# Kernel tuning notes

Measured on AMD Instinct MI355X. Metric: run time of the kernel, lower is better.

Reference implementation:

```python
import jax, jax.numpy as jnp
import numpy as np

D = 1024      # total input features
R = 32        # number of ragged regions
RMAX = 32     # max region size (padding target)
HIDDEN = [128, 128]
H1, H2 = HIDDEN
B = 8192      # batch size


def _made_masks(r, rmax, hidden):
    """TFP AutoregressiveNetwork masks (left-to-right order, 'equal' hidden degrees,
    params=2, use_bias=False), zero-padded to rmax features."""
    order = np.arange(1, r + 1)
    degs = [order]
    for u in hidden:
        mn = min(int(degs[-1].min()), r - 1)
        degs.append(np.maximum(mn, np.ceil(np.arange(1, u + 1) * (r - 1) / float(u + 1)).astype(np.int64)))
    m1 = np.zeros((rmax, hidden[0]), bool)
    m1[:r] = degs[0][:, None] <= degs[1][None, :]
    m2 = degs[1][:, None] <= degs[2][None, :]
    mout = np.zeros((hidden[-1], rmax * 2), bool)
    out_deg = np.repeat(order, 2)  # output layout is feature-major: [feat, param]
    mout[:, :2 * r] = degs[-1][:, None] < out_deg[None, :]
    return m1, m2, mout


def setup_inputs() -> dict:
    rng = np.random.default_rng(0)
    perm = rng.permutation(D)
    sizes = rng.integers(8, RMAX + 1, size=R)
    idx = np.zeros((R, RMAX), np.int64)
    valid = np.zeros((R, RMAX), bool)
    M1 = np.zeros((R, RMAX, H1), bool)
    M2 = np.zeros((R, H1, H2), bool)
    Mout = np.zeros((R, H2, RMAX * 2), bool)
    pos = 0
    for i in range(R):
        s = int(sizes[i])
        idx[i, :s] = perm[pos:pos + s]
        pos += s
        valid[i, :s] = True
        M1[i], M2[i], Mout[i] = _made_masks(s, RMAX, HIDDEN)
    key = jax.random.key(0)
    k1, k2, k3, k4 = jax.random.split(key, 4)
    inputs = jax.random.normal(k1, (B, D), jnp.float32)
    W1 = jax.random.normal(k2, (R, RMAX, H1), jnp.float32) / np.float32(np.sqrt(RMAX))
    W2 = jax.random.normal(k3, (R, H1, H2), jnp.float32) / np.float32(np.sqrt(H1))
    Wout = jax.random.normal(k4, (R, H2, RMAX * 2), jnp.float32) / np.float32(np.sqrt(H2))
    return {"inputs": inputs, "W1": W1, "W2": W2, "Wout": Wout,
            "idx": jnp.asarray(idx), "valid": jnp.asarray(valid),
            "M1": jnp.asarray(M1), "M2": jnp.asarray(M2), "Mout": jnp.asarray(Mout)}


def reference(inputs, W1, W2, Wout, idx, valid, M1, M2, Mout):
    f = inputs.dtype
    v = valid.astype(f)                              # [R, RMAX]
    xg = jnp.take(inputs, idx, axis=1) * v           # [B, R, RMAX] ragged gather (padded)
    # MADE masked MLP (relu, no bias), batched over all regions at once
    h1 = jax.nn.relu(jnp.einsum('brd,rdh->brh', xg, W1 * M1.astype(f)))
    h2 = jax.nn.relu(jnp.einsum('brh,rhk->brk', h1, W2 * M2.astype(f)))
    out = jnp.einsum('brk,rko->bro', h2, Wout * Mout.astype(f))
    out = out.reshape(out.shape[0], out.shape[1], RMAX, 2)
    shift, log_s = out[..., 0], out[..., 1]
    # MAF inverse: u = (x - shift) * exp(-log_scale); logdet = -sum(log_scale)
    u = (xg - shift) * jnp.exp(-log_s)
    elem = -0.5 * u * u - 0.5 * jnp.log(2.0 * jnp.pi) - log_s
    ll = jnp.sum(elem * v, axis=-1)                  # [B, R]
    return ll[..., None]                             # [B, R, 1] as in tf.stack of expand_dims
```

## Files before the change

### kernel.cpp

```cpp
#include <hip/hip_runtime.h>
#include <math.h>


#define RR 32
#define DD 1024
#define HH 128
#define OO 64
#define TROWS 64
#define TILES 8
#define BLOCKS_PER_R 16

#define SHP 136
#define SXG 40
#define SSC 136

typedef _Float16 f16x8_t __attribute__((ext_vector_type(8)));
typedef float f32x4_t __attribute__((ext_vector_type(4)));
typedef unsigned short u16;
typedef unsigned int u32;

__device__ __forceinline__ u32 pkrtz(float a, float b) {
    union { __fp16 v __attribute__((ext_vector_type(2))); u32 u; } c;
    c.v = __builtin_amdgcn_cvt_pkrtz(a, b);
    return c.u;
}
__device__ __forceinline__ f32x4_t mfma16h(f16x8_t a, f16x8_t b, f32x4_t c) {
    return __builtin_amdgcn_mfma_f32_16x16x32_f16(a, b, c, 0, 0, 0);
}

__device__ __forceinline__ void stage_block16(const float* __restrict__ W,
                                              const int* __restrict__ M,
                                              int ldc, int c0, int K, u16* dst,
                                              int tid)
{
    const int kb = tid >> 3;
    const int cb = tid & 7;
    if (kb * 4 >= K) return;
    const int k0 = kb * 4;
    float e[4][4];
#pragma unroll
    for (int i = 0; i < 4; ++i) {
        const int o = ((k0 + i) * ldc + c0 + 4 * cb) >> 2;
        float4 w = ((const float4*)W)[o];
        int4   m = ((const int4*)M)[o];
        e[i][0] = m.x ? w.x : 0.f; e[i][1] = m.y ? w.y : 0.f;
        e[i][2] = m.z ? w.z : 0.f; e[i][3] = m.w ? w.w : 0.f;
    }
#pragma unroll
    for (int j = 0; j < 4; ++j) {
        uint2 p;
        p.x = pkrtz(e[0][j], e[1][j]);
        p.y = pkrtz(e[2][j], e[3][j]);
        *(uint2*)&dst[(4 * cb + j) * SSC + k0] = p;
    }
}

__device__ __forceinline__ void relu_store16(u16* __restrict__ dst, int o, f32x4_t a)
{
    uint2 s;
    s.x = pkrtz(fmaxf(a[0], 0.f), fmaxf(a[1], 0.f));
    s.y = pkrtz(fmaxf(a[2], 0.f), fmaxf(a[3], 0.f));
    *(uint2*)&dst[o] = s;
}

__global__ __launch_bounds__(512, 4)
void made_flow_r26(const float* __restrict__ inputs,
                   const float* __restrict__ W1,
                   const float* __restrict__ W2,
                   const float* __restrict__ Wout,
                   const int* __restrict__ idx,
                   const int* __restrict__ valid,
                   const int* __restrict__ M1,
                   const int* __restrict__ M2,
                   const int* __restrict__ Mout,
                   float* __restrict__ out)
{
    __shared__ __align__(16) u16 h1s[TROWS * SHP];
    __shared__ __align__(16) u16 h2s[TROWS * SHP];
    __shared__ __align__(16) u16 wout_lds[OO * SSC];
    __shared__ __align__(16) u16 xgh[2][TROWS * SXG];
    __shared__ __align__(16) float red2[2][TROWS][4];
    __shared__ int   idx_s[RR];
    __shared__ float v_s[RR];

    u16* const scr  = h1s;
    u16* const scr2 = h2s;

    const int tid  = threadIdx.x;
    const int r    = blockIdx.x / BLOCKS_PER_R;
    const int rb   = blockIdx.x % BLOCKS_PER_R;
    const int ts64 = rb * TILES * TROWS;

    const int lane = tid & 63;
    const int wave = tid >> 6;
    const int q    = lane >> 4;
    const int l16  = lane & 15;
    const int mq   = wave & 3;
    const int nh   = wave >> 2;
    const int wm3  = wave & 3;
    const int ni3  = wave >> 2;

    if (tid < RR) {
        idx_s[tid] = idx[r * RR + tid];
        v_s[tid]   = valid[r * RR + tid] ? 1.f : 0.f;
    }

    f16x8_t a1[2];
    f16x8_t a2[2][4];
    {
        const float* W1r = W1 + r * RR * HH;   const int* M1r = M1 + r * RR * HH;
        const float* W2r = W2 + r * HH * HH;   const int* M2r = M2 + r * HH * HH;
        const float* Wor = Wout + r * HH * OO; const int* Mor = Mout + r * HH * OO;
        for (int i = 0; i < 2; ++i) {
            __syncthreads();
            if (tid < 256) stage_block16(W2r, M2r, HH, 32 * (2 * i),     HH, scr,  tid);
            else           stage_block16(W2r, M2r, HH, 32 * (2 * i + 1), HH, scr2, tid - 256);
            __syncthreads();
            if (mq == 2 * i) {
#pragma unroll
                for (int mi = 0; mi < 2; ++mi)
#pragma unroll
                    for (int ks = 0; ks < 4; ++ks)
                        a2[mi][ks] = *(const f16x8_t*)&scr[(16 * mi + l16) * SSC + ks * 32 + q * 8];
            } else if (mq == 2 * i + 1) {
#pragma unroll
                for (int mi = 0; mi < 2; ++mi)
#pragma unroll
                    for (int ks = 0; ks < 4; ++ks)
                        a2[mi][ks] = *(const f16x8_t*)&scr2[(16 * mi + l16) * SSC + ks * 32 + q * 8];
            }
        }
        for (int i = 0; i < 2; ++i) {
            __syncthreads();
            if (tid < 256) stage_block16(W1r, M1r, HH, 32 * (2 * i),     RR, scr,  tid);
            else           stage_block16(W1r, M1r, HH, 32 * (2 * i + 1), RR, scr2, tid - 256);
            __syncthreads();
            if (mq == 2 * i) {
#pragma unroll
                for (int mi = 0; mi < 2; ++mi)
                    a1[mi] = *(const f16x8_t*)&scr [(16 * mi + l16) * SSC + q * 8];
            } else if (mq == 2 * i + 1) {
#pragma unroll
                for (int mi = 0; mi < 2; ++mi)
                    a1[mi] = *(const f16x8_t*)&scr2[(16 * mi + l16) * SSC + q * 8];
            }
        }
        if (tid < 256) stage_block16(Wor, Mor, OO, 0,  HH, wout_lds,            tid);
        else           stage_block16(Wor, Mor, OO, 32, HH, wout_lds + 32 * SSC, tid - 256);
    }
    __syncthreads();

    const f32x4_t zero4 = {0.f, 0.f, 0.f, 0.f};
    const int grow = tid >> 4;
    const int gg   = tid & 15;
    const int   ci0 = idx_s[2 * gg], ci1 = idx_s[2 * gg + 1];
    const float cv0 = v_s[2 * gg],   cv1 = v_s[2 * gg + 1];
    const int j0  = 8 * wm3 + 2 * q;
    const float vj0 = v_s[j0], vj1 = v_s[j0 + 1];
    const int gb0 = (ts64 + grow) * DD;
    const int gb1 = (ts64 + 32 + grow) * DD;

    float gx[4];
    {
        float a0 = inputs[gb0 + ci0] * cv0, a1v = inputs[gb0 + ci1] * cv1;
        float b0 = inputs[gb1 + ci0] * cv0, b1v = inputs[gb1 + ci1] * cv1;
        *(u32*)&xgh[0][grow * SXG + 2 * gg]        = pkrtz(a0, a1v);
        *(u32*)&xgh[0][(grow + 32) * SXG + 2 * gg] = pkrtz(b0, b1v);
        gx[0] = inputs[gb0 + TROWS * DD + ci0] * cv0;
        gx[1] = inputs[gb0 + TROWS * DD + ci1] * cv1;
        gx[2] = inputs[gb1 + TROWS * DD + ci0] * cv0;
        gx[3] = inputs[gb1 + TROWS * DD + ci1] * cv1;
    }
    __syncthreads();

    {
#pragma unroll
        for (int nn = 0; nn < 2; ++nn) {
            const int rw = 16 * (2 * nh + nn) + l16;
            f16x8_t b = *(const f16x8_t*)&xgh[0][rw * SXG + q * 8];
#pragma unroll
            for (int mi = 0; mi < 2; ++mi) {
                f32x4_t a = mfma16h(a1[mi], b, zero4);
                relu_store16(h1s, rw * SHP + 32 * mq + 16 * mi + 4 * q, a);
            }
        }
    }

    for (int t = 0; t < TILES; ++t) {
        __syncthreads();

        const bool dg = (t + 1 < TILES);

        if (dg) {
            *(u32*)&xgh[(t + 1) & 1][grow * SXG + 2 * gg]        = pkrtz(gx[0], gx[1]);
            *(u32*)&xgh[(t + 1) & 1][(grow + 32) * SXG + 2 * gg] = pkrtz(gx[2], gx[3]);
        }
        if (t + 2 < TILES) {
            const int base = (t + 2) * (TROWS * DD);
            gx[0] = inputs[gb0 + base + ci0] * cv0;
            gx[1] = inputs[gb0 + base + ci1] * cv1;
            gx[2] = inputs[gb1 + base + ci0] * cv0;
            gx[3] = inputs[gb1 + base + ci1] * cv1;
        }
        {
            f32x4_t acc[2][2] = {{zero4, zero4}, {zero4, zero4}};
            __builtin_amdgcn_s_setprio(1);
#pragma unroll
            for (int ks = 0; ks < 4; ++ks) {
#pragma unroll
                for (int nn = 0; nn < 2; ++nn) {
                    f16x8_t b = *(const f16x8_t*)&h1s[(16 * (2 * nh + nn) + l16) * SHP + ks * 32 + q * 8];
#pragma unroll
                    for (int mi = 0; mi < 2; ++mi)
                        acc[mi][nn] = mfma16h(a2[mi][ks], b, acc[mi][nn]);
                }
            }
            __builtin_amdgcn_s_setprio(0);
#pragma unroll
            for (int mi = 0; mi < 2; ++mi)
#pragma unroll
                for (int nn = 0; nn < 2; ++nn)
                    relu_store16(h2s, (16 * (2 * nh + nn) + l16) * SHP + 32 * mq + 16 * mi + 4 * q,
                                 acc[mi][nn]);
        }
        if (t >= 2 && tid < TROWS) {
            float4 rv = *(const float4*)&red2[t & 1][tid][0];
            out[((rb * TILES + (t - 2)) * TROWS + tid) * RR + r] =
                rv.x + rv.y + rv.z + rv.w;
        }
        __syncthreads();

        f32x4_t acc3[2] = {zero4, zero4};
        __builtin_amdgcn_s_setprio(1);
#pragma unroll
        for (int ks = 0; ks < 4; ++ks) {
            f16x8_t ao = *(const f16x8_t*)&wout_lds[(16 * wm3 + l16) * SSC + ks * 32 + q * 8];
#pragma unroll
            for (int nn = 0; nn < 2; ++nn) {
                f16x8_t b = *(const f16x8_t*)&h2s[(16 * (ni3 + 2 * nn) + l16) * SHP + ks * 32 + q * 8];
                acc3[nn] = mfma16h(ao, b, acc3[nn]);
            }
        }
        __builtin_amdgcn_s_setprio(0);

        if (dg) {
#pragma unroll
            for (int nn = 0; nn < 2; ++nn) {
                const int rw = 16 * (2 * nh + nn) + l16;
                f16x8_t b = *(const f16x8_t*)&xgh[(t + 1) & 1][rw * SXG + q * 8];
#pragma unroll
                for (int mi = 0; mi < 2; ++mi) {
                    f32x4_t a = mfma16h(a1[mi], b, zero4);
                    relu_store16(h1s, rw * SHP + 32 * mq + 16 * mi + 4 * q, a);
                }
            }
        }

#pragma unroll
        for (int nn = 0; nn < 2; ++nn) {
            const int row = 16 * (ni3 + 2 * nn) + l16;
            u32 xw = *(const u32*)&xgh[t & 1][row * SXG + j0];
            union { u32 u; _Float16 h[2]; } xc; xc.u = xw;
            const float xv0 = (float)xc.h[0], xv1 = (float)xc.h[1];
            f32x4_t a = acc3[nn];
            const float u0 = (xv0 - a[0]) * __expf(-a[1]);
            const float u1 = (xv1 - a[2]) * __expf(-a[3]);
            float p = (-0.5f * u0 * u0 - 0.91893853320467266954f - a[1]) * vj0
                    + (-0.5f * u1 * u1 - 0.91893853320467266954f - a[3]) * vj1;
            p += __shfl_xor(p, 16, 64);
            p += __shfl_xor(p, 32, 64);
            if (q == 0) red2[t & 1][row][wm3] = p;
        }
    }

    __syncthreads();
    if (tid < 2 * TROWS) {
        const int tt  = TILES - 2 + (tid >> 6);
        const int row = tid & 63;
        float4 rv = *(const float4*)&red2[tt & 1][row][0];
        out[((rb * TILES + tt) * TROWS + row) * RR + r] =
            rv.x + rv.y + rv.z + rv.w;
    }
}

extern "C" void kernel_launch(void* const* d_in, const int* in_sizes, int n_in,
                              void* d_out, int out_size, void* d_ws, size_t ws_size,
                              hipStream_t stream)
{
    const float* inputs = (const float*)d_in[0];
    const float* W1     = (const float*)d_in[1];
    const float* W2     = (const float*)d_in[2];
    const float* Wout   = (const float*)d_in[3];
    const int*   idx    = (const int*)d_in[4];
    const int*   valid  = (const int*)d_in[5];
    const int*   M1     = (const int*)d_in[6];
    const int*   M2     = (const int*)d_in[7];
    const int*   Mout   = (const int*)d_in[8];
    float*       out    = (float*)d_out;

    hipLaunchKernelGGL(made_flow_r26, dim3(RR * BLOCKS_PER_R), dim3(512), 0, stream,
                       inputs, W1, W2, Wout, idx, valid, M1, M2, Mout, out);
}
```

Before: 118.9 us.

## Restructure weight staging prologue and hoist gathers ahead of weight loads

```diff
diff --git a/kernel.cpp b/kernel.cpp
--- a/kernel.cpp
+++ b/kernel.cpp
@@ -13,6 +13,7 @@
 #define SHP 136
 #define SXG 40
 #define SSC 136
+#define SW1 40
 
 typedef _Float16 f16x8_t __attribute__((ext_vector_type(8)));
 typedef float f32x4_t __attribute__((ext_vector_type(4)));
@@ -30,11 +31,11 @@
 
 __device__ __forceinline__ void stage_block16(const float* __restrict__ W,
                                               const int* __restrict__ M,
-                                              int ldc, int c0, int K, u16* dst,
-                                              int tid)
+                                              int ldc, int c0, int K,
+                                              u16* dst, int sd, int tp)
 {
-    const int kb = tid >> 3;
-    const int cb = tid & 7;
+    const int kb = tp >> 3;
+    const int cb = tp & 7;
     if (kb * 4 >= K) return;
     const int k0 = kb * 4;
     float e[4][4];
@@ -51,7 +52,7 @@
         uint2 p;
         p.x = pkrtz(e[0][j], e[1][j]);
         p.y = pkrtz(e[2][j], e[3][j]);
-        *(uint2*)&dst[(4 * cb + j) * SSC + k0] = p;
+        *(uint2*)&dst[(4 * cb + j) * sd + k0] = p;
     }
 }
 
@@ -64,7 +65,7 @@
 }
 
 __global__ __launch_bounds__(512, 4)
-void made_flow_r26(const float* __restrict__ inputs,
+void made_flow_r27(const float* __restrict__ inputs,
                    const float* __restrict__ W1,
                    const float* __restrict__ W2,
                    const float* __restrict__ Wout,
@@ -80,11 +81,10 @@
     __shared__ __align__(16) u16 wout_lds[OO * SSC];
     __shared__ __align__(16) u16 xgh[2][TROWS * SXG];
     __shared__ __align__(16) float red2[2][TROWS][4];
-    __shared__ int   idx_s[RR];
-    __shared__ float v_s[RR];
 
     u16* const scr  = h1s;
     u16* const scr2 = h2s;
+    u16* const xw1  = &xgh[0][0];
 
     const int tid  = threadIdx.x;
     const int r    = blockIdx.x / BLOCKS_PER_R;
@@ -100,10 +100,27 @@
     const int wm3  = wave & 3;
     const int ni3  = wave >> 2;
 
-    if (tid < RR) {
-        idx_s[tid] = idx[r * RR + tid];
-        v_s[tid]   = valid[r * RR + tid] ? 1.f : 0.f;
-    }
+    const int grow = tid >> 4;
+    const int gg   = tid & 15;
+    const int   ci0 = idx[r * RR + 2 * gg];
+    const int   ci1 = idx[r * RR + 2 * gg + 1];
+    const float cv0 = valid[r * RR + 2 * gg]     ? 1.f : 0.f;
+    const float cv1 = valid[r * RR + 2 * gg + 1] ? 1.f : 0.f;
+    const int j0  = 8 * wm3 + 2 * q;
+    const float vj0 = valid[r * RR + j0]     ? 1.f : 0.f;
+    const float vj1 = valid[r * RR + j0 + 1] ? 1.f : 0.f;
+    const int gb0 = (ts64 + grow) * DD;
+    const int gb1 = (ts64 + 32 + grow) * DD;
+
+    float g0[4], gx[4];
+    g0[0] = inputs[gb0 + ci0] * cv0;
+    g0[1] = inputs[gb0 + ci1] * cv1;
+    g0[2] = inputs[gb1 + ci0] * cv0;
+    g0[3] = inputs[gb1 + ci1] * cv1;
+    gx[0] = inputs[gb0 + TROWS * DD + ci0] * cv0;
+    gx[1] = inputs[gb0 + TROWS * DD + ci1] * cv1;
+    gx[2] = inputs[gb1 + TROWS * DD + ci0] * cv0;
+    gx[3] = inputs[gb1 + TROWS * DD + ci1] * cv1;
 
     f16x8_t a1[2];
     f16x8_t a2[2][4];
@@ -111,66 +128,58 @@
         const float* W1r = W1 + r * RR * HH;   const int* M1r = M1 + r * RR * HH;
         const float* W2r = W2 + r * HH * HH;   const int* M2r = M2 + r * HH * HH;
         const float* Wor = Wout + r * HH * OO; const int* Mor = Mout + r * HH * OO;
-        for (int i = 0; i < 2; ++i) {
-            __syncthreads();
-            if (tid < 256) stage_block16(W2r, M2r, HH, 32 * (2 * i),     HH, scr,  tid);
-            else           stage_block16(W2r, M2r, HH, 32 * (2 * i + 1), HH, scr2, tid - 256);
-            __syncthreads();
-            if (mq == 2 * i) {
-#pragma unroll
-                for (int mi = 0; mi < 2; ++mi)
-#pragma unroll
-                    for (int ks = 0; ks < 4; ++ks)
-                        a2[mi][ks] = *(const f16x8_t*)&scr[(16 * mi + l16) * SSC + ks * 32 + q * 8];
-            } else if (mq == 2 * i + 1) {
-#pragma unroll
-                for (int mi = 0; mi < 2; ++mi)
-#pragma unroll
-                    for (int ks = 0; ks < 4; ++ks)
-                        a2[mi][ks] = *(const f16x8_t*)&scr2[(16 * mi + l16) * SSC + ks * 32 + q * 8];
-            }
-        }
-        for (int i = 0; i < 2; ++i) {
-            __syncthreads();
-            if (tid < 256) stage_block16(W1r, M1r, HH, 32 * (2 * i),     RR, scr,  tid);
-            else           stage_block16(W1r, M1r, HH, 32 * (2 * i + 1), RR, scr2, tid - 256);
-            __syncthreads();
-            if (mq == 2 * i) {
-#pragma unroll
-                for (int mi = 0; mi < 2; ++mi)
-                    a1[mi] = *(const f16x8_t*)&scr [(16 * mi + l16) * SSC + q * 8];
-            } else if (mq == 2 * i + 1) {
-#pragma unroll
-                for (int mi = 0; mi < 2; ++mi)
-                    a1[mi] = *(const f16x8_t*)&scr2[(16 * mi + l16) * SSC + q * 8];
-            }
-        }
-        if (tid < 256) stage_block16(Wor, Mor, OO, 0,  HH, wout_lds,            tid);
-        else           stage_block16(Wor, Mor, OO, 32, HH, wout_lds + 32 * SSC, tid - 256);
-    }
-    __syncthreads();
+
+        if (tid < 256) stage_block16(W2r, M2r, HH, 0,  HH, scr,  SSC, tid);
+        else           stage_block16(W2r, M2r, HH, 32, HH, scr2, SSC, tid - 256);
+        __syncthreads();
+        if (mq == 0) {
+#pragma unroll
+            for (int mi = 0; mi < 2; ++mi)
+#pragma unroll
+                for (int ks = 0; ks < 4; ++ks)
+                    a2[mi][ks] = *(const f16x8_t*)&scr[(16 * mi + l16) * SSC + ks * 32 + q * 8];
+        } else if (mq == 1) {
+#pragma unroll
+            for (int mi = 0; mi < 2; ++mi)
+#pragma unroll
+                for (int ks = 0; ks < 4; ++ks)
+                    a2[mi][ks] = *(const f16x8_t*)&scr2[(16 * mi + l16) * SSC + ks * 32 + q * 8];
+        }
+        if (tid < 256) stage_block16(Wor, Mor, OO, 0,  HH, wout_lds,            SSC, tid);
+        else           stage_block16(Wor, Mor, OO, 32, HH, wout_lds + 32 * SSC, SSC, tid - 256);
+        __syncthreads();
+        if (tid < 256) stage_block16(W2r, M2r, HH, 64, HH, scr,  SSC, tid);
+        else           stage_block16(W2r, M2r, HH, 96, HH, scr2, SSC, tid - 256);
+        __syncthreads();
+        if (mq == 2) {
+#pragma unroll
+            for (int mi = 0; mi < 2; ++mi)
+#pragma unroll
+                for (int ks = 0; ks < 4; ++ks)
+                    a2[mi][ks] = *(const f16x8_t*)&scr[(16 * mi + l16) * SSC + ks * 32 + q * 8];
+        } else if (mq == 3) {
+#pragma unroll
+            for (int mi = 0; mi < 2; ++mi)
+#pragma unroll
+                for (int ks = 0; ks < 4; ++ks)
+                    a2[mi][ks] = *(const f16x8_t*)&scr2[(16 * mi + l16) * SSC + ks * 32 + q * 8];
+        }
+        if (tid < 256) {
+            const int c  = tid >> 6;
+            const int tp = tid & 63;
+            stage_block16(W1r, M1r, HH, 32 * c, RR, xw1 + 32 * c * SW1, SW1, tp);
+        }
+        __syncthreads();
+#pragma unroll
+        for (int mi = 0; mi < 2; ++mi)
+            a1[mi] = *(const f16x8_t*)&xw1[(32 * mq + 16 * mi + l16) * SW1 + q * 8];
+        __syncthreads();
+    }
 
     const f32x4_t zero4 = {0.f, 0.f, 0.f, 0.f};
-    const int grow = tid >> 4;
-    const int gg   = tid & 15;
-    const int   ci0 = idx_s[2 * gg], ci1 = idx_s[2 * gg + 1];
-    const float cv0 = v_s[2 * gg],   cv1 = v_s[2 * gg + 1];
-    const int j0  = 8 * wm3 + 2 * q;
-    const float vj0 = v_s[j0], vj1 = v_s[j0 + 1];
-    const int gb0 = (ts64 + grow) * DD;
-    const int gb1 = (ts64 + 32 + grow) * DD;
-
-    float gx[4];
-    {
-        float a0 = inputs[gb0 + ci0] * cv0, a1v = inputs[gb0 + ci1] * cv1;
-        float b0 = inputs[gb1 + ci0] * cv0, b1v = inputs[gb1 + ci1] * cv1;
-        *(u32*)&xgh[0][grow * SXG + 2 * gg]        = pkrtz(a0, a1v);
-        *(u32*)&xgh[0][(grow + 32) * SXG + 2 * gg] = pkrtz(b0, b1v);
-        gx[0] = inputs[gb0 + TROWS * DD + ci0] * cv0;
-        gx[1] = inputs[gb0 + TROWS * DD + ci1] * cv1;
-        gx[2] = inputs[gb1 + TROWS * DD + ci0] * cv0;
-        gx[3] = inputs[gb1 + TROWS * DD + ci1] * cv1;
-    }
+
+    *(u32*)&xgh[0][grow * SXG + 2 * gg]        = pkrtz(g0[0], g0[1]);
+    *(u32*)&xgh[0][(grow + 32) * SXG + 2 * gg] = pkrtz(g0[2], g0[3]);
     __syncthreads();
 
     {
@@ -195,6 +204,34 @@
             *(u32*)&xgh[(t + 1) & 1][grow * SXG + 2 * gg]        = pkrtz(gx[0], gx[1]);
             *(u32*)&xgh[(t + 1) & 1][(grow + 32) * SXG + 2 * gg] = pkrtz(gx[2], gx[3]);
         }
+        {
+            f32x4_t acc[2][2] = {{zero4, zero4}, {zero4, zero4}};
+            __builtin_amdgcn_s_setprio(1);
+#pragma unroll
+            for (int ks = 0; ks < 4; ++ks) {
+#pragma unroll
+                for (int nn = 0; nn < 2; ++nn) {
+                    f16x8_t b = *(const f16x8_t*)&h1s[(16 * (2 * nh + nn) + l16) * SHP + ks * 32 + q * 8];
+#pragma unroll
+                    for (int mi = 0; mi < 2; ++mi)
+                        acc[mi][nn] = mfma16h(a2[mi][ks], b, acc[mi][nn]);
+                }
+            }
+            __builtin_amdgcn_s_setprio(0);
+#pragma unroll
+            for (int mi = 0; mi < 2; ++mi)
+#pragma unroll
+                for (int nn = 0; nn < 2; ++nn)
+                    relu_store16(h2s, (16 * (2 * nh + nn) + l16) * SHP + 32 * mq + 16 * mi + 4 * q,
+                                 acc[mi][nn]);
+        }
+        if (t >= 2 && tid < TROWS) {
+            float4 rv = *(const float4*)&red2[t & 1][tid][0];
+            out[((rb * TILES + (t - 2)) * TROWS + tid) * RR + r] =
+                rv.x + rv.y + rv.z + rv.w;
+        }
+        __syncthreads();
+
         if (t + 2 < TILES) {
             const int base = (t + 2) * (TROWS * DD);
             gx[0] = inputs[gb0 + base + ci0] * cv0;
@@ -202,33 +239,11 @@
             gx[2] = inputs[gb1 + base + ci0] * cv0;
             gx[3] = inputs[gb1 + base + ci1] * cv1;
         }
-        {
-            f32x4_t acc[2][2] = {{zero4, zero4}, {zero4, zero4}};
-            __builtin_amdgcn_s_setprio(1);
-#pragma unroll
-            for (int ks = 0; ks < 4; ++ks) {
-#pragma unroll
-                for (int nn = 0; nn < 2; ++nn) {
-                    f16x8_t b = *(const f16x8_t*)&h1s[(16 * (2 * nh + nn) + l16) * SHP + ks * 32 + q * 8];
-#pragma unroll
-                    for (int mi = 0; mi < 2; ++mi)
-                        acc[mi][nn] = mfma16h(a2[mi][ks], b, acc[mi][nn]);
-                }
-            }
-            __builtin_amdgcn_s_setprio(0);
-#pragma unroll
-            for (int mi = 0; mi < 2; ++mi)
-#pragma unroll
-                for (int nn = 0; nn < 2; ++nn)
-                    relu_store16(h2s, (16 * (2 * nh + nn) + l16) * SHP + 32 * mq + 16 * mi + 4 * q,
-                                 acc[mi][nn]);
-        }
-        if (t >= 2 && tid < TROWS) {
-            float4 rv = *(const float4*)&red2[t & 1][tid][0];
-            out[((rb * TILES + (t - 2)) * TROWS + tid) * RR + r] =
-                rv.x + rv.y + rv.z + rv.w;
-        }
-        __syncthreads();
+
+        u32 xw[2];
+#pragma unroll
+        for (int nn = 0; nn < 2; ++nn)
+            xw[nn] = *(const u32*)&xgh[t & 1][(16 * (ni3 + 2 * nn) + l16) * SXG + j0];
 
         f32x4_t acc3[2] = {zero4, zero4};
         __builtin_amdgcn_s_setprio(1);
@@ -259,8 +274,7 @@
 #pragma unroll
         for (int nn = 0; nn < 2; ++nn) {
             const int row = 16 * (ni3 + 2 * nn) + l16;
-            u32 xw = *(const u32*)&xgh[t & 1][row * SXG + j0];
-            union { u32 u; _Float16 h[2]; } xc; xc.u = xw;
+            union { u32 u; _Float16 h[2]; } xc; xc.u = xw[nn];
             const float xv0 = (float)xc.h[0], xv1 = (float)xc.h[1];
             f32x4_t a = acc3[nn];
             const float u0 = (xv0 - a[0]) * __expf(-a[1]);
@@ -298,6 +312,6 @@
     const int*   Mout   = (const int*)d_in[8];
     float*       out    = (float*)d_out;
 
-    hipLaunchKernelGGL(made_flow_r26, dim3(RR * BLOCKS_PER_R), dim3(512), 0, stream,
+    hipLaunchKernelGGL(made_flow_r27, dim3(RR * BLOCKS_PER_R), dim3(512), 0, stream,
                        inputs, W1, W2, Wout, idx, valid, M1, M2, Mout, out);
 }
```

Result: no change. 117.1 us (-1.6%).
